# Kernel optimization log

Measured on AMD Instinct MI355X. Metric: run time of the kernel, lower is better.

Reference implementation:

```python
import jax, jax.numpy as jnp
import numpy as np

D_STATE = 8
DT_RANK = 8  # ceil(128/16)


def _grouped_1x1(x, w):
    # x: (B,H,W,Cin), w: (g, Cout//g, Cin//g)
    B, H, W, _ = x.shape
    g, o, i = w.shape
    xg = x.reshape(B, H, W, g, i)
    return jnp.einsum('bhwgi,goi->bhwgo', xg, w).reshape(B, H, W, g * o)


def setup_inputs() -> dict:
    key = jax.random.key(0)
    ks = jax.random.split(key, 16)
    B, H, W, C = 8, 64, 64, 128
    g = 4
    D = 128  # expand_dim = d_inner
    N = D_STATE
    R = DT_RANK
    inp = {}
    inp['x'] = jax.random.normal(ks[0], (B, H, W, C), dtype=jnp.float32)
    inp['w1'] = jax.random.normal(ks[1], (g, D // g, C // g), dtype=jnp.float32) * 0.1
    inp['dw'] = jax.random.normal(ks[2], (3, 3, 1, D), dtype=jnp.float32) * 0.1  # HWIO depthwise
    inp['in_proj_w'] = jax.random.normal(ks[3], (2 * D, D), dtype=jnp.float32) * 0.05
    inp['conv1d_w'] = jax.random.normal(ks[4], (D, 3), dtype=jnp.float32) * 0.1
    inp['conv1d_b'] = jax.random.normal(ks[5], (D,), dtype=jnp.float32) * 0.05
    inp['x_proj_w'] = jax.random.normal(ks[6], (R + 2 * N, D), dtype=jnp.float32) * 0.05
    inp['dt_proj_w'] = jax.random.normal(ks[7], (D, R), dtype=jnp.float32) * 0.05
    inp['dt_proj_b'] = jax.random.normal(ks[8], (D,), dtype=jnp.float32) * 0.05
    inp['A_log'] = jnp.log(jnp.tile(jnp.arange(1, N + 1, dtype=jnp.float32)[None, :], (D, 1)))
    inp['D_param'] = jnp.ones((D,), dtype=jnp.float32)
    inp['out_proj_w'] = jax.random.normal(ks[9], (D, D), dtype=jnp.float32) * 0.05
    inp['gamma'] = jnp.ones((D,), dtype=jnp.float32)
    inp['beta'] = jnp.zeros((D,), dtype=jnp.float32)
    inp['w2'] = jax.random.normal(ks[10], (g, D // g, C // g), dtype=jnp.float32) * 0.1
    inp['wout'] = jax.random.normal(ks[11], (g, C // g, D // g), dtype=jnp.float32) * 0.1
    return inp


def _mamba(x_seq, in_proj_w, conv1d_w, conv1d_b, x_proj_w, dt_proj_w, dt_proj_b, A_log, D_param, out_proj_w):
    # x_seq: (B, L, D)
    B, L, D = x_seq.shape
    N, R = D_STATE, DT_RANK
    xz = jnp.einsum('bld,ed->ble', x_seq, in_proj_w)  # (B,L,2D)
    u, z = xz[..., :D], xz[..., D:]
    # causal depthwise conv1d, kernel=3, left pad 2 (torch: padding=2, slice [:L])
    up = jnp.pad(u, ((0, 0), (2, 0), (0, 0)))
    u = (up[:, 0:L] * conv1d_w[:, 0] + up[:, 1:L + 1] * conv1d_w[:, 1]
         + up[:, 2:L + 2] * conv1d_w[:, 2] + conv1d_b)
    u = jax.nn.silu(u)
    x_dbl = jnp.einsum('bld,ed->ble', u, x_proj_w)  # (B,L,R+2N)
    dt = x_dbl[..., :R]
    Bm = x_dbl[..., R:R + N]
    Cm = x_dbl[..., R + N:]
    delta = jax.nn.softplus(jnp.einsum('blr,dr->bld', dt, dt_proj_w) + dt_proj_b)  # (B,L,D)
    A = -jnp.exp(A_log)  # (D,N)

    def step(h, inp):
        d_t, u_t, b_t, c_t = inp  # (B,D),(B,D),(B,N),(B,N)
        dA = jnp.exp(d_t[..., None] * A)            # (B,D,N)
        h = dA * h + (d_t * u_t)[..., None] * b_t[:, None, :]
        y_t = jnp.einsum('bdn,bn->bd', h, c_t)
        return h, y_t

    h0 = jnp.zeros((B, D, N), dtype=x_seq.dtype)
    xs = (jnp.swapaxes(delta, 0, 1), jnp.swapaxes(u, 0, 1),
          jnp.swapaxes(Bm, 0, 1), jnp.swapaxes(Cm, 0, 1))
    _, ys = jax.lax.scan(step, h0, xs)              # ys: (L,B,D)
    y = jnp.swapaxes(ys, 0, 1) + u * D_param
    y = y * jax.nn.silu(z)
    return jnp.einsum('bld,ed->ble', y, out_proj_w)


def reference(x, w1, dw, in_proj_w, conv1d_w, conv1d_b, x_proj_w, dt_proj_w, dt_proj_b,
              A_log, D_param, out_proj_w, gamma, beta, w2, wout):
    B, H, W, C = x.shape
    D = dw.shape[-1]
    x1 = _grouped_1x1(x, w1)  # (B,H,W,D)
    x1 = jax.lax.conv_general_dilated(
        x1, dw, window_strides=(1, 1), padding='SAME',
        feature_group_count=D, dimension_numbers=('NHWC', 'HWIO', 'NHWC'))
    x1 = jax.nn.silu(x1)
    x1_seq = x1.reshape(B, H * W, D)
    x1_seq = _mamba(x1_seq, in_proj_w, conv1d_w, conv1d_b, x_proj_w,
                    dt_proj_w, dt_proj_b, A_log, D_param, out_proj_w)
    x1 = x1_seq.reshape(B, H, W, D)
    mu = jnp.mean(x1, axis=-1, keepdims=True)
    var = jnp.mean(jnp.square(x1 - mu), axis=-1, keepdims=True)
    x1 = (x1 - mu) * jax.lax.rsqrt(var + 1e-5) * gamma + beta
    x2 = jax.nn.silu(_grouped_1x1(x, w2))
    x_fuse = x1 * x2
    return _grouped_1x1(x_fuse, wout)  # (B,H,W,C)
```

## Files before the change

kernel.cpp:

```cpp
#include <hip/hip_runtime.h>
#include <math.h>

#define B_    8
#define C_    128
#define D_    128
#define L_    4096
#define NPOS_ 32768
#define NC_   256
#define S_    16
#define MFL_  1048576

typedef __attribute__((ext_vector_type(8))) short short8;
typedef __attribute__((ext_vector_type(4))) float f32x4;

__device__ __forceinline__ float siluf(float x) { return x / (1.f + __expf(-x)); }
__device__ __forceinline__ float softplusf(float x) {
    if (x > 20.f) return x;
    return __logf(1.f + __expf(x));
}
__device__ __forceinline__ unsigned short f2bf(float f) {
    unsigned int u = __float_as_uint(f);
    u = (u + 0x7FFFu + ((u >> 16) & 1u)) >> 16;
    return (unsigned short)u;
}
__device__ __forceinline__ float bf2f(unsigned short h) {
    return __uint_as_float(((unsigned int)h) << 16);
}
__device__ __forceinline__ void scan_as(float dl, const float* Ar, bool fast, float* a) {
    if (fast) {
        float e1 = __expf(-dl);
        a[0] = e1;
        a[1] = e1 * e1;
        a[2] = a[1] * e1;
        a[3] = a[1] * a[1];
        a[4] = a[3] * e1;
        a[5] = a[3] * a[1];
        a[6] = a[5] * e1;
        a[7] = a[3] * a[3];
    } else {
        #pragma unroll
        for (int n = 0; n < 8; ++n) a[n] = __expf(dl * Ar[n]);
    }
}

__global__ __launch_bounds__(256) void k1_g1x1(const float* __restrict__ x,
                                               const float* __restrict__ w1,
                                               const float* __restrict__ w2,
                                               const float* __restrict__ inW,
                                               const float* __restrict__ OW,
                                               const float* __restrict__ xpw,
                                               unsigned short* __restrict__ inWb,
                                               unsigned short* __restrict__ OWb,
                                               unsigned short* __restrict__ xpwb,
                                               unsigned short* __restrict__ t1b,
                                               unsigned short* __restrict__ x2sb) {
    __shared__ float xs[16 * 128];
    int t = threadIdx.x;
    {
        int i = blockIdx.x * 51 + t;
        if (t < 51 && i < 52224) {
            if (i < 32768)      inWb[i] = f2bf(inW[i]);
            else if (i < 49152) OWb[i - 32768] = f2bf(OW[i - 32768]);
            else                xpwb[i - 49152] = f2bf(xpw[i - 49152]);
        }
    }
    int d = t & 127, ph = t >> 7;
    int g = d >> 5, o = d & 31;
    float w1r[32], w2r[32];
    #pragma unroll
    for (int i = 0; i < 32; ++i) {
        w1r[i] = w1[g * 1024 + o * 32 + i];
        w2r[i] = w2[g * 1024 + o * 32 + i];
    }
    int pos0 = blockIdx.x * 32;
    for (int it = 0; it < 2; ++it) {
        int p0 = pos0 + it * 16;
        #pragma unroll
        for (int q = 0; q < 2; ++q) {
            int fi = t * 2 + q;
            *(float4*)&xs[fi * 4] = *(const float4*)&x[p0 * 128 + fi * 4];
        }
        __syncthreads();
        #pragma unroll
        for (int q = 0; q < 8; ++q) {
            int pl = ph * 8 + q;
            float a1 = 0.f, a2 = 0.f;
            const float* xr = &xs[pl * 128 + g * 32];
            #pragma unroll
            for (int i4 = 0; i4 < 8; ++i4) {
                float4 xv = *(const float4*)&xr[i4 * 4];
                a1 += xv.x * w1r[i4*4] + xv.y * w1r[i4*4+1] + xv.z * w1r[i4*4+2] + xv.w * w1r[i4*4+3];
                a2 += xv.x * w2r[i4*4] + xv.y * w2r[i4*4+1] + xv.z * w2r[i4*4+2] + xv.w * w2r[i4*4+3];
            }
            int pos = p0 + pl;
            t1b[pos * 128 + d]  = f2bf(a1);
            x2sb[pos * 128 + d] = f2bf(siluf(a2));
        }
        __syncthreads();
    }
}

__global__ __launch_bounds__(128) void k2_dwconv(const unsigned short* __restrict__ t1b,
                                                 const float* __restrict__ dw,
                                                 unsigned short* __restrict__ x1cb) {
    int d = threadIdx.x;
    float dwr[9];
    #pragma unroll
    for (int k = 0; k < 9; ++k) dwr[k] = dw[k * 128 + d];
    int bid = blockIdx.x;
    int wt = bid & 15, ht = (bid >> 4) & 7, b = bid >> 7;
    int h0 = ht * 8, w0 = wt * 4;
    float rows[10][6];
    #pragma unroll
    for (int r = 0; r < 10; ++r) {
        int hh = h0 - 1 + r;
        bool hv = (hh >= 0) && (hh < 64);
        #pragma unroll
        for (int c = 0; c < 6; ++c) {
            int w = w0 - 1 + c;
            bool wvv = (w >= 0) && (w < 64);
            rows[r][c] = (hv && wvv) ? bf2f(t1b[((b * 64 + hh) * 64 + w) * 128 + d]) : 0.f;
        }
    }
    #pragma unroll
    for (int hi = 0; hi < 8; ++hi) {
        #pragma unroll
        for (int wi = 0; wi < 4; ++wi) {
            float acc = rows[hi][wi]     * dwr[0] + rows[hi][wi+1]   * dwr[1] + rows[hi][wi+2]   * dwr[2]
                      + rows[hi+1][wi]   * dwr[3] + rows[hi+1][wi+1] * dwr[4] + rows[hi+1][wi+2] * dwr[5]
                      + rows[hi+2][wi]   * dwr[6] + rows[hi+2][wi+1] * dwr[7] + rows[hi+2][wi+2] * dwr[8];
            x1cb[((b * 64 + h0 + hi) * 64 + w0 + wi) * 128 + d] = f2bf(siluf(acc));
        }
    }
}

__global__ __launch_bounds__(256) void k3_mfma(const unsigned short* __restrict__ Abf,
                                               const unsigned short* __restrict__ Bbf,
                                               unsigned short* __restrict__ urawb,
                                               unsigned short* __restrict__ zb) {
    __shared__ unsigned short Al[64 * 72];
    __shared__ unsigned short Bl[128 * 72];
    int t = threadIdx.x;
    int pos0 = (blockIdx.x >> 1) * 64;
    int half = blockIdx.x & 1;
    const unsigned short* Bh = Bbf + (size_t)half * 128 * 128;
    unsigned short* dst = half ? zb : urawb;
    int lane = t & 63, wv = t >> 6;
    int lanem = lane & 15, laneq = lane >> 4;
    f32x4 acc[8];
    #pragma unroll
    for (int i = 0; i < 8; ++i) acc[i] = (f32x4){0.f, 0.f, 0.f, 0.f};
    for (int kc = 0; kc < 2; ++kc) {
        #pragma unroll
        for (int q = 0; q < 2; ++q) {
            int c = t + q * 256;
            int row = c >> 3, col = c & 7;
            *(int4*)&Al[row * 72 + col * 8] = *(const int4*)&Abf[(pos0 + row) * 128 + kc * 64 + col * 8];
        }
        #pragma unroll
        for (int q = 0; q < 4; ++q) {
            int c = t + q * 256;
            int row = c >> 3, col = c & 7;
            *(int4*)&Bl[row * 72 + col * 8] = *(const int4*)&Bh[row * 128 + kc * 64 + col * 8];
        }
        __syncthreads();
        #pragma unroll
        for (int ks = 0; ks < 2; ++ks) {
            short8 af = *(const short8*)&Al[(wv * 16 + lanem) * 72 + ks * 32 + laneq * 8];
            #pragma unroll
            for (int ni = 0; ni < 8; ++ni) {
                short8 bfr = *(const short8*)&Bl[(ni * 16 + lanem) * 72 + ks * 32 + laneq * 8];
                acc[ni] = __builtin_amdgcn_mfma_f32_16x16x32_bf16(af, bfr, acc[ni], 0, 0, 0);
            }
        }
        __syncthreads();
    }
    #pragma unroll
    for (int ni = 0; ni < 8; ++ni)
        #pragma unroll
        for (int r = 0; r < 4; ++r) {
            int m = pos0 + wv * 16 + laneq * 4 + r;
            int n = ni * 16 + lanem;
            dst[m * 128 + n] = f2bf(acc[ni][r]);
        }
}

__global__ __launch_bounds__(256) void k45_convproj(const unsigned short* __restrict__ urawb,
                                                    const float* __restrict__ cw,
                                                    const float* __restrict__ cb,
                                                    const unsigned short* __restrict__ xpwb,
                                                    const float* __restrict__ dtw,
                                                    const float* __restrict__ dtb,
                                                    const float* __restrict__ A_log,
                                                    unsigned short* __restrict__ usb,
                                                    unsigned short* __restrict__ deltab,
                                                    float* __restrict__ Bm,
                                                    float* __restrict__ Cm,
                                                    float* __restrict__ cA,
                                                    float* __restrict__ cB) {
    __shared__ unsigned short uA[32 * 136];
    __shared__ unsigned short xB[32 * 136];
    __shared__ float xdb[32 * 36];
    int t = threadIdx.x;
    int d = t & 127, ph = t >> 7;
    for (int i = t; i < 32 * 128; i += 256) {
        int n = i >> 7, k = i & 127;
        xB[n * 136 + k] = (n < 24) ? xpwb[n * 128 + k] : (unsigned short)0;
    }
    float cw0 = cw[d * 3 + 0], cw1 = cw[d * 3 + 1], cw2 = cw[d * 3 + 2], cbr = cb[d];
    float dtwr[8];
    #pragma unroll
    for (int r = 0; r < 8; ++r) dtwr[r] = dtw[d * 8 + r];
    float dtbr = dtb[d];
    float Ar[8]; bool fast = true;
    #pragma unroll
    for (int n = 0; n < 8; ++n) {
        Ar[n] = -__expf(A_log[d * 8 + n]);
        fast = fast && (fabsf(Ar[n] + (float)(n + 1)) < 2e-3f);
    }

    int gpos0 = blockIdx.x * 32;
    int ll0 = (gpos0 & 4095) + ph * 16;
    int base = (gpos0 + ph * 16) * 128 + d;
    float ur0 = (ll0 >= 2) ? bf2f(urawb[base - 256]) : 0.f;
    float ur1 = (ll0 >= 1) ? bf2f(urawb[base - 128]) : 0.f;
    #pragma unroll
    for (int q = 0; q < 16; ++q) {
        float urq = bf2f(urawb[base + q * 128]);
        float v = siluf(ur0 * cw0 + ur1 * cw1 + urq * cw2 + cbr);
        unsigned short vb = f2bf(v);
        usb[base + q * 128] = vb;
        uA[(ph * 16 + q) * 136 + d] = vb;
        ur0 = ur1; ur1 = urq;
    }
    __syncthreads();
    int lane = t & 63, wv = t >> 6;
    int lanem = lane & 15, laneq = lane >> 4;
    int m0 = (wv & 1) * 16, n0 = (wv >> 1) * 16;
    f32x4 accx = (f32x4){0.f, 0.f, 0.f, 0.f};
    #pragma unroll
    for (int ks = 0; ks < 4; ++ks) {
        short8 af  = *(const short8*)&uA[(m0 + lanem) * 136 + ks * 32 + laneq * 8];
        short8 bfr = *(const short8*)&xB[(n0 + lanem) * 136 + ks * 32 + laneq * 8];
        accx = __builtin_amdgcn_mfma_f32_16x16x32_bf16(af, bfr, accx, 0, 0, 0);
    }
    #pragma unroll
    for (int r = 0; r < 4; ++r)
        xdb[(m0 + laneq * 4 + r) * 36 + n0 + lanem] = accx[r];
    __syncthreads();
    float h[8], ap[8];
    #pragma unroll
    for (int n = 0; n < 8; ++n) { h[n] = 0.f; ap[n] = 1.f; }
    #pragma unroll
    for (int q = 0; q < 16; ++q) {
        int pl = ph * 16 + q;
        float dt = dtbr;
        #pragma unroll
        for (int r = 0; r < 8; ++r) dt += xdb[pl * 36 + r] * dtwr[r];
        unsigned short dlb = f2bf(softplusf(dt));
        deltab[base + q * 128] = dlb;
        float dl = bf2f(dlb);
        float du = dl * bf2f(uA[pl * 136 + d]);
        float a[8];
        scan_as(dl, Ar, fast, a);
        #pragma unroll
        for (int n = 0; n < 8; ++n) {
            ap[n] *= a[n];
            h[n] = a[n] * h[n] + du * xdb[pl * 36 + 8 + n];
        }
    }
    int bH = gpos0 >> 12;
    int c  = ((gpos0 & 4095) >> 4) + ph;
    int obase = ((bH * NC_ + c) * 128 + d) * 8;
    *(float4*)&cA[obase]     = make_float4(ap[0], ap[1], ap[2], ap[3]);
    *(float4*)&cA[obase + 4] = make_float4(ap[4], ap[5], ap[6], ap[7]);
    *(float4*)&cB[obase]     = make_float4(h[0], h[1], h[2], h[3]);
    *(float4*)&cB[obase + 4] = make_float4(h[4], h[5], h[6], h[7]);
    for (int i = t; i < 512; i += 256) {
        int p = i >> 4, j = i & 15;
        float v = xdb[p * 36 + 8 + j];
        int gp = gpos0 + p;
        if (j < 8) Bm[gp * 8 + j] = v;
        else       Cm[gp * 8 + (j - 8)] = v;
    }
}

__global__ __launch_bounds__(128) void k6_scan2(const float* __restrict__ cA,
                                                const float* __restrict__ cB,
                                                float* __restrict__ carry) {
    int b = blockIdx.x >> 3;
    int slice = blockIdx.x & 7;
    int dn = slice * 128 + threadIdx.x;
    float h = 0.f;
    #pragma unroll 8
    for (int c = 0; c < NC_; ++c) {
        int idx = (b * NC_ + c) * 1024 + dn;
        float a  = cA[idx];
        float bv = cB[idx];
        carry[idx] = h;
        h = a * h + bv;
    }
}

__global__ __launch_bounds__(256) void k7f_fused(const unsigned short* __restrict__ deltab,
                                                 const unsigned short* __restrict__ usb,
                                                 const float* __restrict__ Bm,
                                                 const float* __restrict__ Cm,
                                                 const unsigned short* __restrict__ zb,
                                                 const float* __restrict__ A_log,
                                                 const float* __restrict__ Dp,
                                                 const float* __restrict__ carry,
                                                 const unsigned short* __restrict__ OWb,
                                                 const float* __restrict__ gamma,
                                                 const float* __restrict__ beta,
                                                 const unsigned short* __restrict__ x2sb,
                                                 const float* __restrict__ wout,
                                                 float* __restrict__ out) {
    __shared__ __align__(16) char smem[37888];
    unsigned short* yA = (unsigned short*)smem;
    unsigned short* Bl = (unsigned short*)(smem + 18432);
    float* xz = (float*)smem;
    __shared__ float woutL[4 * 1160];
    __shared__ float gbL[256];
    int t = threadIdx.x;
    for (int idx = t; idx < 4096; idx += 256) {
        int g = idx >> 10, r = idx & 1023, o = r >> 5, i = r & 31;
        woutL[g * 1160 + o * 36 + i] = wout[idx];
    }
    if (t < 128) gbL[t] = gamma[t];
    else         gbL[t] = beta[t - 128];

    int d = t & 127, ph = t >> 7;
    int b = blockIdx.x >> 6, cblk = blockIdx.x & 63;
    float Ar[8]; bool fast = true;
    #pragma unroll
    for (int n = 0; n < 8; ++n) {
        Ar[n] = -__expf(A_log[d * 8 + n]);
        fast = fast && (fabsf(Ar[n] + (float)(n + 1)) < 2e-3f);
    }
    float Dpr = Dp[d];
    int ybase = (d >> 6) * (64 * 72) + (d & 63);
    for (int cc = 0; cc < 2; ++cc) {
        int cl = ph * 2 + cc;
        int c = cblk * 4 + cl;
        int cbase = ((b * NC_ + c) * 128 + d) * 8;
        float4 h0 = *(const float4*)&carry[cbase];
        float4 h1 = *(const float4*)&carry[cbase + 4];
        float h[8] = {h0.x, h0.y, h0.z, h0.w, h1.x, h1.y, h1.z, h1.w};
        int base  = (b * L_ + c * S_) * 128 + d;
        int bbase = (b * L_ + c * S_) * 8;
        #pragma unroll
        for (int s = 0; s < S_; ++s) {
            float dl = bf2f(deltab[base + s * 128]);
            float uv = bf2f(usb[base + s * 128]);
            float zv = bf2f(zb[base + s * 128]);
            float du = dl * uv;
            float4 bm0 = *(const float4*)&Bm[bbase + s * 8];
            float4 bm1 = *(const float4*)&Bm[bbase + s * 8 + 4];
            float4 cm0 = *(const float4*)&Cm[bbase + s * 8];
            float4 cm1 = *(const float4*)&Cm[bbase + s * 8 + 4];
            float a[8];
            scan_as(dl, Ar, fast, a);
            h[0] = a[0] * h[0] + du * bm0.x;
            h[1] = a[1] * h[1] + du * bm0.y;
            h[2] = a[2] * h[2] + du * bm0.z;
            h[3] = a[3] * h[3] + du * bm0.w;
            h[4] = a[4] * h[4] + du * bm1.x;
            h[5] = a[5] * h[5] + du * bm1.y;
            h[6] = a[6] * h[6] + du * bm1.z;
            h[7] = a[7] * h[7] + du * bm1.w;
            float yv = h[0] * cm0.x + h[1] * cm0.y + h[2] * cm0.z + h[3] * cm0.w
                     + h[4] * cm1.x + h[5] * cm1.y + h[6] * cm1.z + h[7] * cm1.w;
            yv = (yv + uv * Dpr) * siluf(zv);
            yA[ybase + (cl * 16 + s) * 72] = f2bf(yv);
        }
    }
    __syncthreads();

    int lane = t & 63, wv = t >> 6;
    int lanem = lane & 15, laneq = lane >> 4;
    f32x4 acc[8];
    #pragma unroll
    for (int i = 0; i < 8; ++i) acc[i] = (f32x4){0.f, 0.f, 0.f, 0.f};
    for (int kc = 0; kc < 2; ++kc) {
        #pragma unroll
        for (int q = 0; q < 4; ++q) {
            int cidx = t + q * 256;
            int row = cidx >> 3, col = cidx & 7;
            *(int4*)&Bl[row * 72 + col * 8] = *(const int4*)&OWb[row * 128 + kc * 64 + col * 8];
        }
        __syncthreads();
        #pragma unroll
        for (int ks = 0; ks < 2; ++ks) {
            short8 af = *(const short8*)&yA[kc * (64 * 72) + (wv * 16 + lanem) * 72 + ks * 32 + laneq * 8];
            #pragma unroll
            for (int ni = 0; ni < 8; ++ni) {
                short8 bfr = *(const short8*)&Bl[(ni * 16 + lanem) * 72 + ks * 32 + laneq * 8];
                acc[ni] = __builtin_amdgcn_mfma_f32_16x16x32_bf16(af, bfr, acc[ni], 0, 0, 0);
            }
        }
        __syncthreads();
    }
    #pragma unroll
    for (int ni = 0; ni < 8; ++ni) {
        int ch = ni * 16 + lanem;
        int col = ch + ((ch >> 5) << 2);
        #pragma unroll
        for (int r = 0; r < 4; ++r)
            xz[(wv * 16 + laneq * 4 + r) * 148 + col] = bf2f(f2bf(acc[ni][r]));
    }
    __syncthreads();

    int g = t & 3, pos = t >> 2;
    int gpos = b * L_ + cblk * 64 + pos;
    const float* xrow0 = &xz[pos * 148 + g * 36];
    float v[32];
    #pragma unroll
    for (int i4 = 0; i4 < 8; ++i4) {
        float4 xv = *(const float4*)&xrow0[i4 * 4];
        v[i4*4+0] = xv.x; v[i4*4+1] = xv.y;
        v[i4*4+2] = xv.z; v[i4*4+3] = xv.w;
    }
    float s = 0.f, s2 = 0.f;
    #pragma unroll
    for (int i = 0; i < 32; ++i) { s += v[i]; s2 += v[i] * v[i]; }
    s  += __shfl_xor(s, 1, 64);  s  += __shfl_xor(s, 2, 64);
    s2 += __shfl_xor(s2, 1, 64); s2 += __shfl_xor(s2, 2, 64);
    float m = s * (1.f / 128.f);
    float var = s2 * (1.f / 128.f) - m * m;
    float rstd = rsqrtf(var + 1e-5f);
    #pragma unroll
    for (int i4 = 0; i4 < 8; ++i4) {
        ushort4 xv = *(const ushort4*)&x2sb[gpos * 128 + g * 32 + i4 * 4];
        unsigned short xa[4] = {xv.x, xv.y, xv.z, xv.w};
        #pragma unroll
        for (int k = 0; k < 4; ++k) {
            int e = g * 32 + i4 * 4 + k;
            float vv = (v[i4 * 4 + k] - m) * rstd * gbL[e] + gbL[128 + e];
            v[i4 * 4 + k] = vv * bf2f(xa[k]);
        }
    }

    const float* wg = &woutL[g * 1160];
    int obase = gpos * 128 + g * 32;
    #pragma unroll
    for (int ob = 0; ob < 8; ++ob) {
        float o4[4];
        #pragma unroll
        for (int oo = 0; oo < 4; ++oo) {
            int o = ob * 4 + oo;
            float acc2 = 0.f;
            #pragma unroll
            for (int i4 = 0; i4 < 8; ++i4) {
                float4 wv4 = *(const float4*)&wg[o * 36 + i4 * 4];
                acc2 += v[i4*4] * wv4.x + v[i4*4+1] * wv4.y
                      + v[i4*4+2] * wv4.z + v[i4*4+3] * wv4.w;
            }
            o4[oo] = acc2;
        }
        *(float4*)&out[obase + ob * 4] = make_float4(o4[0], o4[1], o4[2], o4[3]);
    }
}

extern "C" void kernel_launch(void* const* d_in, const int* in_sizes, int n_in,
                              void* d_out, int out_size, void* d_ws, size_t ws_size,
                              hipStream_t stream) {
    (void)in_sizes; (void)n_in; (void)out_size; (void)ws_size;
    const float* x         = (const float*)d_in[0];
    const float* w1        = (const float*)d_in[1];
    const float* dw        = (const float*)d_in[2];
    const float* in_proj_w = (const float*)d_in[3];
    const float* conv1d_w  = (const float*)d_in[4];
    const float* conv1d_b  = (const float*)d_in[5];
    const float* x_proj_w  = (const float*)d_in[6];
    const float* dt_proj_w = (const float*)d_in[7];
    const float* dt_proj_b = (const float*)d_in[8];
    const float* A_log     = (const float*)d_in[9];
    const float* D_param   = (const float*)d_in[10];
    const float* out_proj_w= (const float*)d_in[11];
    const float* gamma     = (const float*)d_in[12];
    const float* beta      = (const float*)d_in[13];
    const float* w2        = (const float*)d_in[14];
    const float* wout      = (const float*)d_in[15];
    float* out = (float*)d_out;

    float* ws = (float*)d_ws;
    unsigned short* x2sb   = (unsigned short*)(ws);
    unsigned short* t1b    = (unsigned short*)(ws + 2  * (size_t)MFL_);
    unsigned short* x1cb   = (unsigned short*)(ws + 4  * (size_t)MFL_);
    unsigned short* urawb  = (unsigned short*)(ws + 6  * (size_t)MFL_);
    unsigned short* zb     = (unsigned short*)(ws + 8  * (size_t)MFL_);
    unsigned short* usb    = (unsigned short*)(ws + 14 * (size_t)MFL_);
    unsigned short* deltab = (unsigned short*)(ws + 16 * (size_t)MFL_);
    float* Bm    = ws + 18 * (size_t)MFL_;
    float* Cm    = Bm + (size_t)NPOS_ * 8;
    float* cA    = Cm + (size_t)NPOS_ * 8;
    float* cB    = cA + 2 * (size_t)MFL_;
    float* carry = cB + 2 * (size_t)MFL_;
    unsigned short* inWb = (unsigned short*)(carry + 2 * (size_t)MFL_);
    unsigned short* OWb  = inWb + 32768;
    unsigned short* xpwb = OWb + 16384;

    k1_g1x1<<<1024, 256, 0, stream>>>(x, w1, w2, in_proj_w, out_proj_w, x_proj_w,
                                      inWb, OWb, xpwb, t1b, x2sb);
    k2_dwconv<<<1024, 128, 0, stream>>>(t1b, dw, x1cb);
    k3_mfma<<<1024, 256, 0, stream>>>(x1cb, inWb, urawb, zb);
    k45_convproj<<<1024, 256, 0, stream>>>(urawb, conv1d_w, conv1d_b, xpwb,
                                           dt_proj_w, dt_proj_b, A_log,
                                           usb, deltab, Bm, Cm, cA, cB);
    k6_scan2<<<64, 128, 0, stream>>>(cA, cB, carry);
    k7f_fused<<<512, 256, 0, stream>>>(deltab, usb, Bm, Cm, zb, A_log, D_param,
                                       carry, OWb, gamma, beta, x2sb, wout, out);
}
```

Baseline: 212.9 us.

## Split sequential chunk-carry scan into two-level parallel scan; vectorize k1 and k45 accesses

```diff
diff --git a/kernel.cpp b/kernel.cpp
--- a/kernel.cpp
+++ b/kernel.cpp
@@ -64,14 +64,13 @@
             else                xpwb[i - 49152] = f2bf(xpw[i - 49152]);
         }
     }
-    int d = t & 127, ph = t >> 7;
-    int g = d >> 5, o = d & 31;
-    float w1r[32], w2r[32];
-    #pragma unroll
-    for (int i = 0; i < 32; ++i) {
-        w1r[i] = w1[g * 1024 + o * 32 + i];
-        w2r[i] = w2[g * 1024 + o * 32 + i];
-    }
+    int op = t & 63, ph = t >> 6;
+    int g = op >> 4, o2 = (op & 15) * 2;
+    const float* w1p = &w1[g * 1024 + o2 * 32];
+    const float* w2p = &w2[g * 1024 + o2 * 32];
+    float w1r[64], w2r[64];
+    #pragma unroll
+    for (int i = 0; i < 64; ++i) { w1r[i] = w1p[i]; w2r[i] = w2p[i]; }
     int pos0 = blockIdx.x * 32;
     for (int it = 0; it < 2; ++it) {
         int p0 = pos0 + it * 16;
@@ -82,19 +81,24 @@
         }
         __syncthreads();
         #pragma unroll
-        for (int q = 0; q < 8; ++q) {
-            int pl = ph * 8 + q;
-            float a1 = 0.f, a2 = 0.f;
+        for (int q = 0; q < 4; ++q) {
+            int pl = ph * 4 + q;
+            float a1 = 0.f, b1 = 0.f, a2 = 0.f, b2 = 0.f;
             const float* xr = &xs[pl * 128 + g * 32];
             #pragma unroll
             for (int i4 = 0; i4 < 8; ++i4) {
                 float4 xv = *(const float4*)&xr[i4 * 4];
-                a1 += xv.x * w1r[i4*4] + xv.y * w1r[i4*4+1] + xv.z * w1r[i4*4+2] + xv.w * w1r[i4*4+3];
-                a2 += xv.x * w2r[i4*4] + xv.y * w2r[i4*4+1] + xv.z * w2r[i4*4+2] + xv.w * w2r[i4*4+3];
+                a1 += xv.x * w1r[i4*4]    + xv.y * w1r[i4*4+1]    + xv.z * w1r[i4*4+2]    + xv.w * w1r[i4*4+3];
+                b1 += xv.x * w1r[32+i4*4] + xv.y * w1r[32+i4*4+1] + xv.z * w1r[32+i4*4+2] + xv.w * w1r[32+i4*4+3];
+                a2 += xv.x * w2r[i4*4]    + xv.y * w2r[i4*4+1]    + xv.z * w2r[i4*4+2]    + xv.w * w2r[i4*4+3];
+                b2 += xv.x * w2r[32+i4*4] + xv.y * w2r[32+i4*4+1] + xv.z * w2r[32+i4*4+2] + xv.w * w2r[32+i4*4+3];
             }
             int pos = p0 + pl;
-            t1b[pos * 128 + d]  = f2bf(a1);
-            x2sb[pos * 128 + d] = f2bf(siluf(a2));
+            int db = pos * 128 + g * 32 + o2;
+            unsigned int u1 = (unsigned int)f2bf(a1) | ((unsigned int)f2bf(b1) << 16);
+            unsigned int u2 = (unsigned int)f2bf(siluf(a2)) | ((unsigned int)f2bf(siluf(b2)) << 16);
+            *(unsigned int*)&t1b[db]  = u1;
+            *(unsigned int*)&x2sb[db] = u2;
         }
         __syncthreads();
     }
@@ -254,19 +258,24 @@
     #pragma unroll
     for (int q = 0; q < 16; ++q) {
         int pl = ph * 16 + q;
-        float dt = dtbr;
-        #pragma unroll
-        for (int r = 0; r < 8; ++r) dt += xdb[pl * 36 + r] * dtwr[r];
+        const float* xrow = &xdb[pl * 36];
+        float4 d0 = *(const float4*)&xrow[0];
+        float4 d1 = *(const float4*)&xrow[4];
+        float dt = dtbr + d0.x * dtwr[0] + d0.y * dtwr[1] + d0.z * dtwr[2] + d0.w * dtwr[3]
+                        + d1.x * dtwr[4] + d1.y * dtwr[5] + d1.z * dtwr[6] + d1.w * dtwr[7];
         unsigned short dlb = f2bf(softplusf(dt));
         deltab[base + q * 128] = dlb;
         float dl = bf2f(dlb);
         float du = dl * bf2f(uA[pl * 136 + d]);
+        float bmv[8];
+        *(float4*)&bmv[0] = *(const float4*)&xrow[8];
+        *(float4*)&bmv[4] = *(const float4*)&xrow[12];
         float a[8];
         scan_as(dl, Ar, fast, a);
         #pragma unroll
         for (int n = 0; n < 8; ++n) {
             ap[n] *= a[n];
-            h[n] = a[n] * h[n] + du * xdb[pl * 36 + 8 + n];
+            h[n] = a[n] * h[n] + du * bmv[n];
         }
     }
     int bH = gpos0 >> 12;
@@ -276,29 +285,54 @@
     *(float4*)&cA[obase + 4] = make_float4(ap[4], ap[5], ap[6], ap[7]);
     *(float4*)&cB[obase]     = make_float4(h[0], h[1], h[2], h[3]);
     *(float4*)&cB[obase + 4] = make_float4(h[4], h[5], h[6], h[7]);
-    for (int i = t; i < 512; i += 256) {
-        int p = i >> 4, j = i & 15;
-        float v = xdb[p * 36 + 8 + j];
+    if (t < 128) {
+        int p = t >> 2, q = t & 3;
+        float4 v = *(const float4*)&xdb[p * 36 + 8 + q * 4];
         int gp = gpos0 + p;
-        if (j < 8) Bm[gp * 8 + j] = v;
-        else       Cm[gp * 8 + (j - 8)] = v;
-    }
-}
-
-__global__ __launch_bounds__(128) void k6_scan2(const float* __restrict__ cA,
-                                                const float* __restrict__ cB,
-                                                float* __restrict__ carry) {
-    int b = blockIdx.x >> 3;
-    int slice = blockIdx.x & 7;
-    int dn = slice * 128 + threadIdx.x;
-    float h = 0.f;
-    #pragma unroll 8
-    for (int c = 0; c < NC_; ++c) {
-        int idx = (b * NC_ + c) * 1024 + dn;
+        if (q < 2) *(float4*)&Bm[gp * 8 + q * 4] = v;
+        else       *(float4*)&Cm[gp * 8 + (q - 2) * 4] = v;
+    }
+}
+
+__global__ __launch_bounds__(256) void k6a_scan(float* __restrict__ cA,
+                                                float* __restrict__ cB,
+                                                float* __restrict__ AgA,
+                                                float* __restrict__ AgB) {
+    int id = blockIdx.x * 256 + threadIdx.x;
+    int dn = id & 1023;
+    int grp = (id >> 10) & 15;
+    int b = id >> 14;
+    float Apre = 1.f, h = 0.f;
+    int base = (b * NC_ + grp * 16) * 1024 + dn;
+    #pragma unroll 4
+    for (int j = 0; j < 16; ++j) {
+        int idx = base + j * 1024;
         float a  = cA[idx];
         float bv = cB[idx];
-        carry[idx] = h;
+        cA[idx] = Apre;
+        cB[idx] = h;
+        Apre *= a;
         h = a * h + bv;
+    }
+    int aidx = (b * 16 + grp) * 1024 + dn;
+    AgA[aidx] = Apre;
+    AgB[aidx] = h;
+}
+
+__global__ __launch_bounds__(256) void k6b_scan(const float* __restrict__ AgA,
+                                                const float* __restrict__ AgB,
+                                                float* __restrict__ gcar) {
+    int id = blockIdx.x * 256 + threadIdx.x;
+    int dn = id & 1023;
+    int b = id >> 10;
+    float h = 0.f;
+    #pragma unroll
+    for (int grp = 0; grp < 16; ++grp) {
+        int idx = (b * 16 + grp) * 1024 + dn;
+        float Ag = AgA[idx];
+        float Bg = AgB[idx];
+        gcar[idx] = h;
+        h = Ag * h + Bg;
     }
 }
 
@@ -309,7 +343,9 @@
                                                  const unsigned short* __restrict__ zb,
                                                  const float* __restrict__ A_log,
                                                  const float* __restrict__ Dp,
-                                                 const float* __restrict__ carry,
+                                                 const float* __restrict__ Apre,
+                                                 const float* __restrict__ Bpre,
+                                                 const float* __restrict__ gcar,
                                                  const unsigned short* __restrict__ OWb,
                                                  const float* __restrict__ gamma,
                                                  const float* __restrict__ beta,
@@ -344,9 +380,17 @@
         int cl = ph * 2 + cc;
         int c = cblk * 4 + cl;
         int cbase = ((b * NC_ + c) * 128 + d) * 8;
-        float4 h0 = *(const float4*)&carry[cbase];
-        float4 h1 = *(const float4*)&carry[cbase + 4];
-        float h[8] = {h0.x, h0.y, h0.z, h0.w, h1.x, h1.y, h1.z, h1.w};
+        float4 ap0 = *(const float4*)&Apre[cbase];
+        float4 ap1 = *(const float4*)&Apre[cbase + 4];
+        float4 bp0 = *(const float4*)&Bpre[cbase];
+        float4 bp1 = *(const float4*)&Bpre[cbase + 4];
+        int gbase = (b * 16 + (c >> 4)) * 1024 + d * 8;
+        float4 g0 = *(const float4*)&gcar[gbase];
+        float4 g1 = *(const float4*)&gcar[gbase + 4];
+        float h[8] = { fmaf(g0.x, ap0.x, bp0.x), fmaf(g0.y, ap0.y, bp0.y),
+                       fmaf(g0.z, ap0.z, bp0.z), fmaf(g0.w, ap0.w, bp0.w),
+                       fmaf(g1.x, ap1.x, bp1.x), fmaf(g1.y, ap1.y, bp1.y),
+                       fmaf(g1.z, ap1.z, bp1.z), fmaf(g1.w, ap1.w, bp1.w) };
         int base  = (b * L_ + c * S_) * 128 + d;
         int bbase = (b * L_ + c * S_) * 8;
         #pragma unroll
@@ -496,8 +540,11 @@
     float* Cm    = Bm + (size_t)NPOS_ * 8;
     float* cA    = Cm + (size_t)NPOS_ * 8;
     float* cB    = cA + 2 * (size_t)MFL_;
-    float* carry = cB + 2 * (size_t)MFL_;
-    unsigned short* inWb = (unsigned short*)(carry + 2 * (size_t)MFL_);
+    float* scanw = cB + 2 * (size_t)MFL_;
+    float* AgA   = scanw;
+    float* AgB   = scanw + 131072;
+    float* gcar  = scanw + 262144;
+    unsigned short* inWb = (unsigned short*)(scanw + 2 * (size_t)MFL_);
     unsigned short* OWb  = inWb + 32768;
     unsigned short* xpwb = OWb + 16384;
 
@@ -508,7 +555,8 @@
     k45_convproj<<<1024, 256, 0, stream>>>(urawb, conv1d_w, conv1d_b, xpwb,
                                            dt_proj_w, dt_proj_b, A_log,
                                            usb, deltab, Bm, Cm, cA, cB);
-    k6_scan2<<<64, 128, 0, stream>>>(cA, cB, carry);
+    k6a_scan<<<512, 256, 0, stream>>>(cA, cB, AgA, AgB);
+    k6b_scan<<<32, 256, 0, stream>>>(AgA, AgB, gcar);
     k7f_fused<<<512, 256, 0, stream>>>(deltab, usb, Bm, Cm, zb, A_log, D_param,
-                                       carry, OWb, gamma, beta, x2sb, wout, out);
-}
+                                       cA, cB, gcar, OWb, gamma, beta, x2sb, wout, out);
+}
```

Result: no change. 214.9 us (+0.9%).
